# Performance work log

Hardware: AMD Instinct MI355X
Metric: run time of the kernel (lower is better)

The kernel has to match this reference:

```python
import jax, jax.numpy as jnp
import numpy as np

B, C, L, D = 8, 256, 2048, 128  # batch, in_channels, seq_len, n_factor


def setup_inputs() -> dict:
    key = jax.random.key(0)
    ks = jax.random.split(key, 8)
    s = 1.0 / np.sqrt(C)
    return {
        "x_inner": jax.random.normal(ks[0], (B, C, L), jnp.float32),
        "x_outer": jax.random.normal(ks[1], (B, C, L), jnp.float32),
        "Wq": jax.random.normal(ks[2], (D, C), jnp.float32) * s,
        "bq": jax.random.normal(ks[3], (D,), jnp.float32) * 0.01,
        "Wk": jax.random.normal(ks[4], (D, C), jnp.float32) * s,
        "bk": jax.random.normal(ks[5], (D,), jnp.float32) * 0.01,
        "Wv": jax.random.normal(ks[6], (D, C), jnp.float32) * s,
        "bv": jax.random.normal(ks[7], (D,), jnp.float32) * 0.01,
    }


def reference(x_inner, x_outer, Wq, bq, Wk, bk, Wv, bv):
    # kernel-size-1 Conv1d == per-position linear over channels; permute -> [B, L, D]
    q = jnp.einsum('bcl,dc->bld', x_inner, Wq) + bq  # [B, Lq, D]
    k = jnp.einsum('bcl,dc->bld', x_outer, Wk) + bk  # [B, Lk, D]
    v = jnp.einsum('bcl,dc->bld', x_outer, Wv) + bv  # [B, Lk, D]
    scores = jnp.einsum('bqd,bkd->bqk', q, k) / jnp.sqrt(jnp.asarray(D, q.dtype))
    attn = jax.nn.softmax(scores, axis=2)            # [B, Lq, Lk]
    return jnp.einsum('bqk,bkd->bqd', attn, v)       # [B, Lq, D]
```

## Files before the change

### kernel.cpp

```cpp
#include <hip/hip_runtime.h>
#include <hip/hip_bf16.h>

#define NB 8
#define NC 256
#define NL 2048
#define ND 128
#define NROWS (NB * NL)
#define QKV_ELEMS ((size_t)NB * NL * ND)
#define W_ELEMS (ND * NC)
#define XS_STRIDE 264

typedef __attribute__((ext_vector_type(8))) short bf16x8;
typedef __attribute__((ext_vector_type(4))) float f32x4;
typedef __attribute__((ext_vector_type(16))) float f32x16;
typedef __attribute__((ext_vector_type(4))) unsigned int u32x4;

__device__ __forceinline__ unsigned short f2bf(float f) {
    union { float f; unsigned u; } v; v.f = f;
    unsigned r = v.u + 0x7fffu + ((v.u >> 16) & 1u);
    return (unsigned short)(r >> 16);
}

__device__ __forceinline__ unsigned cvt_pk_bf16(float lo, float hi) {
    unsigned r;
    asm("v_cvt_pk_bf16_f32 %0, %1, %2" : "=v"(r) : "v"(lo), "v"(hi));
    return r;
}

__device__ __forceinline__ void pl32swap(unsigned &a, unsigned &b) {
    asm("v_permlane32_swap_b32 %0, %1" : "+v"(a), "+v"(b));
}

__device__ __forceinline__ void load_lds16(const unsigned short* g, unsigned short* l) {
    __builtin_amdgcn_global_load_lds((const __attribute__((address_space(1))) unsigned int*)g,
                                     (__attribute__((address_space(3))) unsigned int*)l, 16, 0, 0);
}

__global__ void cast_w3(const float* __restrict__ wq, const float* __restrict__ wk,
                        const float* __restrict__ wv, unsigned short* __restrict__ dst) {
    int i = blockIdx.x * blockDim.x + threadIdx.x;
    if (i >= 3 * W_ELEMS) return;
    int sel = i / W_ELEMS, off = i - sel * W_ELEMS;
    const float* s = (sel == 0) ? wq : (sel == 1) ? wk : wv;
    dst[i] = f2bf(s[off]);
}

__device__ __forceinline__ int xs_col(int row, int col) {
    return col ^ (((row >> 2) & 7) << 3);
}

__device__ __forceinline__ void qk_project(const unsigned short* xs, const unsigned short* Wb,
                                           const float* bias, unsigned short* out,
                                           int b, int l0, int wave, int ln, int quad) {
    int m0w = wave * 16;
    f32x4 acc[8] = {};
    int rowq = m0w + ln;
    #pragma unroll
    for (int s = 0; s < 8; s++) {
        bf16x8 af = *reinterpret_cast<const bf16x8*>(xs + rowq * XS_STRIDE + xs_col(rowq, s * 32 + quad * 8));
        #pragma unroll
        for (int t = 0; t < 8; t++) {
            bf16x8 bfr = *reinterpret_cast<const bf16x8*>(Wb + (size_t)(t * 16 + ln) * NC + s * 32 + quad * 8);
            acc[t] = __builtin_amdgcn_mfma_f32_16x16x32_bf16(af, bfr, acc[t], 0, 0, 0);
        }
    }
    #pragma unroll
    for (int t = 0; t < 8; t++) {
        int col = t * 16 + ln;
        float bi = bias[col];
        #pragma unroll
        for (int r = 0; r < 4; r++)
            out[(size_t)(b * NL + l0 + m0w + quad * 4 + r) * ND + col] = f2bf(acc[t][r] + bi);
    }
}

__global__ __launch_bounds__(256, 4) void proj_direct(const float* __restrict__ xi,
                                                      const float* __restrict__ xo,
                                                      const unsigned short* __restrict__ Wall,
                                                      const float* __restrict__ bq,
                                                      const float* __restrict__ bk,
                                                      const float* __restrict__ bv,
                                                      unsigned short* __restrict__ Qb,
                                                      unsigned short* __restrict__ Kb,
                                                      unsigned short* __restrict__ Vtb) {
    __shared__ unsigned short xs[64 * XS_STRIDE];
    int b = blockIdx.x >> 5, lt = blockIdx.x & 31, l0 = lt * 64;
    int y = blockIdx.y;
    int wave = threadIdx.x >> 6, lane = threadIdx.x & 63;
    int ln = lane & 15, quad = lane >> 4;

    const float* xsrc = (y == 0 ? xi : xo) + (size_t)b * NC * NL + l0;
    int l4 = ln * 4;
    #pragma unroll
    for (int G = 0; G < 4; G++) {
        int c0 = G * 64 + wave * 16 + quad * 4;
        float4 r[4];
        #pragma unroll
        for (int cc = 0; cc < 4; cc++)
            r[cc] = *reinterpret_cast<const float4*>(xsrc + (size_t)(c0 + cc) * NL + l4);
        #pragma unroll
        for (int k = 0; k < 4; k++) {
            int row = l4 + k;
            const float* f0 = reinterpret_cast<const float*>(&r[0]);
            const float* f1 = reinterpret_cast<const float*>(&r[1]);
            const float* f2 = reinterpret_cast<const float*>(&r[2]);
            const float* f3 = reinterpret_cast<const float*>(&r[3]);
            uint2 w2 = { cvt_pk_bf16(f0[k], f1[k]), cvt_pk_bf16(f2[k], f3[k]) };
            *reinterpret_cast<uint2*>(&xs[row * XS_STRIDE + xs_col(row, c0)]) = w2;
        }
    }
    __syncthreads();

    if (y == 0) {
        qk_project(xs, Wall, bq, Qb, b, l0, wave, ln, quad);
    } else {
        qk_project(xs, Wall + W_ELEMS, bk, Kb, b, l0, wave, ln, quad);
        const unsigned short* Wb = Wall + 2 * (size_t)W_ELEMS;
        f32x4 acc[2][4] = {};
        #pragma unroll
        for (int s = 0; s < 8; s++) {
            bf16x8 wf0 = *reinterpret_cast<const bf16x8*>(Wb + (size_t)(wave * 32 + ln) * NC + s * 32 + quad * 8);
            bf16x8 wf1 = *reinterpret_cast<const bf16x8*>(Wb + (size_t)(wave * 32 + 16 + ln) * NC + s * 32 + quad * 8);
            #pragma unroll
            for (int t = 0; t < 4; t++) {
                int rowv = t * 16 + ln;
                bf16x8 xb = *reinterpret_cast<const bf16x8*>(xs + rowv * XS_STRIDE + xs_col(rowv, s * 32 + quad * 8));
                acc[0][t] = __builtin_amdgcn_mfma_f32_16x16x32_bf16(wf0, xb, acc[0][t], 0, 0, 0);
                acc[1][t] = __builtin_amdgcn_mfma_f32_16x16x32_bf16(wf1, xb, acc[1][t], 0, 0, 0);
            }
        }
        #pragma unroll
        for (int u = 0; u < 2; u++)
            #pragma unroll
            for (int t = 0; t < 4; t++)
                #pragma unroll
                for (int r = 0; r < 4; r++) {
                    int d = wave * 32 + u * 16 + quad * 4 + r;
                    Vtb[(size_t)(b * ND + d) * NL + l0 + t * 16 + ln] = f2bf(acc[u][t][r] + bv[d]);
                }
    }
}

__global__ __launch_bounds__(256, 2) void flash_attn_s2(const unsigned short* __restrict__ Q,
                                                        const unsigned short* __restrict__ K,
                                                        const unsigned short* __restrict__ Vt,
                                                        float* __restrict__ Opart,
                                                        float* __restrict__ lbuf,
                                                        int kvlen) {
    __shared__ unsigned short kbuf[2][64 * 128];
    __shared__ unsigned short vbuf[2][128 * 64];
    int bx = blockIdx.x;
    bx = ((bx & 7) << 5) | (bx >> 3);
    int b = bx >> 5, qt = bx & 31;
    int q0 = qt * 64;
    int sp = blockIdx.y;
    int kv0 = sp * kvlen;
    int wave = threadIdx.x >> 6, lane = threadIdx.x & 63;
    int l31 = lane & 31, h = lane >> 5;
    int qg = wave >> 1, half = wave & 1;
    const float scale = 0.08838834764831845f * 1.4426950408889634f;

    bf16x8 qf[8];
    const unsigned short* qrow = Q + (size_t)(b * NL + q0 + qg * 32 + l31) * ND + h * 8;
    #pragma unroll
    for (int s = 0; s < 8; s++) qf[s] = *reinterpret_cast<const bf16x8*>(qrow + s * 16);

    float lsum = 0.f;
    f32x16 o_acc[4] = {};

    const unsigned short* kg = K + (size_t)b * NL * ND;
    const unsigned short* vg = Vt + (size_t)b * ND * NL;

    int krt = wave * 16 + (lane >> 4);
    int kjs = (lane & 15);
    int vdt = wave * 32 + (lane >> 3);
    int vjs = (lane & 7);

    #pragma unroll
    for (int i = 0; i < 4; i++) {
        int rt = krt + i * 4;
        load_lds16(kg + (size_t)(kv0 + rt) * ND + (kjs ^ (rt & 15)) * 8, kbuf[0] + (wave * 16 + i * 4) * 128);
    }
    #pragma unroll
    for (int i = 0; i < 4; i++) {
        int dt = vdt + i * 8;
        load_lds16(vg + (size_t)dt * NL + kv0 + (vjs ^ (dt & 7)) * 8, vbuf[0] + (wave * 32 + i * 8) * 64);
    }

    int niter = kvlen >> 6;
    for (int it = 0; it < niter; it++) {
        int cur = it & 1;
        __syncthreads();

        if (it + 1 < niter) {
            int kt = kv0 + (it + 1) * 64;
            int nxt = cur ^ 1;
            #pragma unroll
            for (int i = 0; i < 4; i++) {
                int rt = krt + i * 4;
                load_lds16(kg + (size_t)(kt + rt) * ND + (kjs ^ (rt & 15)) * 8, kbuf[nxt] + (wave * 16 + i * 4) * 128);
            }
            #pragma unroll
            for (int i = 0; i < 4; i++) {
                int dt = vdt + i * 8;
                load_lds16(vg + (size_t)dt * NL + kt + (vjs ^ (dt & 7)) * 8, vbuf[nxt] + (wave * 32 + i * 8) * 64);
            }
        }
        const unsigned short* kb = kbuf[cur];
        const unsigned short* vb = vbuf[cur];

        f32x16 sacc0 = {}, sacc1 = {};
        __builtin_amdgcn_s_setprio(1);
        {
            const unsigned short* krow_p = kb + (half * 32 + l31) * 128;
            #pragma unroll
            for (int s = 0; s < 8; s += 2) {
                bf16x8 kf0 = *reinterpret_cast<const bf16x8*>(krow_p + ((((s + 0) * 2 + h) ^ (l31 & 15)) << 3));
                bf16x8 kf1 = *reinterpret_cast<const bf16x8*>(krow_p + ((((s + 1) * 2 + h) ^ (l31 & 15)) << 3));
                sacc0 = __builtin_amdgcn_mfma_f32_32x32x16_bf16(kf0, qf[s], sacc0, 0, 0, 0);
                sacc1 = __builtin_amdgcn_mfma_f32_32x32x16_bf16(kf1, qf[s + 1], sacc1, 0, 0, 0);
            }
        }
        __builtin_amdgcn_s_setprio(0);

        float p[16];
        #pragma unroll
        for (int g = 0; g < 16; g++) p[g] = __builtin_exp2f((sacc0[g] + sacc1[g]) * scale);
        lsum += (((p[0] + p[1]) + (p[2] + p[3])) + ((p[4] + p[5]) + (p[6] + p[7])))
              + (((p[8] + p[9]) + (p[10] + p[11])) + ((p[12] + p[13]) + (p[14] + p[15])));
        unsigned c0 = cvt_pk_bf16(p[0], p[1]),   c1 = cvt_pk_bf16(p[2], p[3]);
        unsigned c2 = cvt_pk_bf16(p[4], p[5]),   c3 = cvt_pk_bf16(p[6], p[7]);
        unsigned c4 = cvt_pk_bf16(p[8], p[9]),   c5 = cvt_pk_bf16(p[10], p[11]);
        unsigned c6 = cvt_pk_bf16(p[12], p[13]), c7 = cvt_pk_bf16(p[14], p[15]);
        pl32swap(c0, c2); pl32swap(c1, c3);
        pl32swap(c4, c6); pl32swap(c5, c7);
        u32x4 wlo = {c0, c1, c2, c3};
        u32x4 whi = {c4, c5, c6, c7};
        bf16x8 pb0 = __builtin_bit_cast(bf16x8, wlo);
        bf16x8 pb1 = __builtin_bit_cast(bf16x8, whi);

        __builtin_amdgcn_s_setprio(1);
        #pragma unroll
        for (int dt = 0; dt < 4; dt++) {
            const unsigned short* vrow = vb + (dt * 32 + l31) * 64;
            int s0 = half * 2;
            bf16x8 vf0 = *reinterpret_cast<const bf16x8*>(vrow + ((((s0 + 0) * 2 + h) ^ (l31 & 7)) << 3));
            bf16x8 vf1 = *reinterpret_cast<const bf16x8*>(vrow + ((((s0 + 1) * 2 + h) ^ (l31 & 7)) << 3));
            o_acc[dt] = __builtin_amdgcn_mfma_f32_32x32x16_bf16(vf0, pb0, o_acc[dt], 0, 0, 0);
            o_acc[dt] = __builtin_amdgcn_mfma_f32_32x32x16_bf16(vf1, pb1, o_acc[dt], 0, 0, 0);
        }
        __builtin_amdgcn_s_setprio(0);
    }
    lsum += __shfl_xor(lsum, 32);

    __syncthreads();
    float* ored = reinterpret_cast<float*>(&kbuf[0][0]);
    float* lred = reinterpret_cast<float*>(&vbuf[0][0]);
    if (half == 1) {
        float* o = ored + qg * (128 * 32);
        #pragma unroll
        for (int dt = 0; dt < 4; dt++)
            #pragma unroll
            for (int g = 0; g < 4; g++)
                #pragma unroll
                for (int r = 0; r < 4; r++)
                    o[(dt * 32 + g * 8 + h * 4 + r) * 32 + l31] = o_acc[dt][g * 4 + r];
        if (lane < 32) lred[qg * 32 + l31] = lsum;
    }
    __syncthreads();
    if (half == 0) {
        float* o = ored + qg * (128 * 32);
        float Lt = lsum + lred[qg * 32 + l31];
        int qrow_g = b * NL + q0 + qg * 32 + l31;
        if (lane < 32) lbuf[(size_t)sp * NROWS + qrow_g] = Lt;
        float* op = Opart + (size_t)sp * QKV_ELEMS;
        #pragma unroll
        for (int dt = 0; dt < 4; dt++) {
            #pragma unroll
            for (int g = 0; g < 4; g++) {
                f32x4 v4;
                #pragma unroll
                for (int r = 0; r < 4; r++)
                    v4[r] = o_acc[dt][g * 4 + r] + o[(dt * 32 + g * 8 + h * 4 + r) * 32 + l31];
                *reinterpret_cast<f32x4*>(op + (size_t)qrow_g * ND + dt * 32 + g * 8 + h * 4) = v4;
            }
        }
    }
}

__global__ __launch_bounds__(256) void attn_merge(const float* __restrict__ Opart,
                                                  const float* __restrict__ lbuf,
                                                  float* __restrict__ out, int S) {
    int idx = blockIdx.x * 256 + threadIdx.x;
    int row = idx >> 5;
    int dg = (idx & 31) * 4;
    float L = 0.f;
    float4 acc = make_float4(0.f, 0.f, 0.f, 0.f);
    for (int s = 0; s < S; s++) {
        L += lbuf[(size_t)s * NROWS + row];
        float4 o = *reinterpret_cast<const float4*>(Opart + (size_t)s * QKV_ELEMS + (size_t)row * ND + dg);
        acc.x += o.x; acc.y += o.y; acc.z += o.z; acc.w += o.w;
    }
    float inv = 1.0f / L;
    float4 res = make_float4(acc.x * inv, acc.y * inv, acc.z * inv, acc.w * inv);
    *reinterpret_cast<float4*>(out + (size_t)row * ND + dg) = res;
}

extern "C" void kernel_launch(void* const* d_in, const int* in_sizes, int n_in,
                              void* d_out, int out_size, void* d_ws, size_t ws_size,
                              hipStream_t stream) {
    const float* x_inner = (const float*)d_in[0];
    const float* x_outer = (const float*)d_in[1];
    const float* Wq = (const float*)d_in[2];
    const float* bq = (const float*)d_in[3];
    const float* Wk = (const float*)d_in[4];
    const float* bk = (const float*)d_in[5];
    const float* Wv = (const float*)d_in[6];
    const float* bv = (const float*)d_in[7];
    float* out = (float*)d_out;

    const int S = 2;
    char* w = (char*)d_ws;
    float* Opart = (float*)w;
    float* lbuf = (float*)(w + (size_t)S * QKV_ELEMS * 4);
    char* w2 = w + (size_t)S * QKV_ELEMS * 4 + (size_t)S * NROWS * 4;
    unsigned short* Qb = (unsigned short*)w2;
    unsigned short* Kb = Qb + QKV_ELEMS;
    unsigned short* Vtb = Kb + QKV_ELEMS;
    unsigned short* Wall = Vtb + QKV_ELEMS;

    cast_w3<<<(3 * W_ELEMS + 255) / 256, 256, 0, stream>>>(Wq, Wk, Wv, Wall);
    dim3 pgrid(NB * (NL / 64), 2);
    proj_direct<<<pgrid, 256, 0, stream>>>(x_inner, x_outer, Wall, bq, bk, bv, Qb, Kb, Vtb);
    dim3 fgrid(NB * (NL / 64), S);
    flash_attn_s2<<<fgrid, 256, 0, stream>>>(Qb, Kb, Vtb, Opart, lbuf, NL / S);
    attn_merge<<<(NROWS * ND / 4 + 255) / 256, 256, 0, stream>>>(Opart, lbuf, out, S);
}
```

Before: 149.0 us.

## Fuse split-KV merge into attention kernel via last-arriver atomic counter

Removes the separate attn_merge kernel. Each attention block writes its partial output and row sums, then bumps a per-tile atomic counter. The second block to arrive reads the other split's partial, normalizes, and writes the final output. The counters are zeroed in the weight-cast kernel. This saves one kernel launch and a full pass over both partial buffers, at the cost of thread fences, an atomic, and extra tail work in the last-arriving blocks.

After: 211.8 us. 42.2% more time.

```diff
diff --git a/kernel.cpp b/kernel.cpp
--- a/kernel.cpp
+++ b/kernel.cpp
@@ -37,8 +37,10 @@
 }
 
 __global__ void cast_w3(const float* __restrict__ wq, const float* __restrict__ wk,
-                        const float* __restrict__ wv, unsigned short* __restrict__ dst) {
+                        const float* __restrict__ wv, unsigned short* __restrict__ dst,
+                        int* __restrict__ cnt) {
     int i = blockIdx.x * blockDim.x + threadIdx.x;
+    if (i < 256) cnt[i] = 0;
     if (i >= 3 * W_ELEMS) return;
     int sel = i / W_ELEMS, off = i - sel * W_ELEMS;
     const float* s = (sel == 0) ? wq : (sel == 1) ? wk : wv;
@@ -146,11 +148,14 @@
                                                         const unsigned short* __restrict__ Vt,
                                                         float* __restrict__ Opart,
                                                         float* __restrict__ lbuf,
+                                                        int* __restrict__ cnt,
+                                                        float* __restrict__ out,
                                                         int kvlen) {
     __shared__ unsigned short kbuf[2][64 * 128];
     __shared__ unsigned short vbuf[2][128 * 64];
-    int bx = blockIdx.x;
-    bx = ((bx & 7) << 5) | (bx >> 3);
+    __shared__ int sOld;
+    int bx_orig = blockIdx.x;
+    int bx = ((bx_orig & 7) << 5) | (bx_orig >> 3);
     int b = bx >> 5, qt = bx & 31;
     int q0 = qt * 64;
     int sp = blockIdx.y;
@@ -268,42 +273,52 @@
         if (lane < 32) lred[qg * 32 + l31] = lsum;
     }
     __syncthreads();
+    int qrow_g = b * NL + q0 + qg * 32 + l31;
+    float Lt = 0.f;
     if (half == 0) {
         float* o = ored + qg * (128 * 32);
-        float Lt = lsum + lred[qg * 32 + l31];
-        int qrow_g = b * NL + q0 + qg * 32 + l31;
+        #pragma unroll
+        for (int dt = 0; dt < 4; dt++)
+            #pragma unroll
+            for (int g = 0; g < 4; g++)
+                #pragma unroll
+                for (int r = 0; r < 4; r++)
+                    o_acc[dt][g * 4 + r] += o[(dt * 32 + g * 8 + h * 4 + r) * 32 + l31];
+        Lt = lsum + lred[qg * 32 + l31];
         if (lane < 32) lbuf[(size_t)sp * NROWS + qrow_g] = Lt;
         float* op = Opart + (size_t)sp * QKV_ELEMS;
         #pragma unroll
         for (int dt = 0; dt < 4; dt++) {
             #pragma unroll
             for (int g = 0; g < 4; g++) {
+                f32x4 v4 = { o_acc[dt][g * 4 + 0], o_acc[dt][g * 4 + 1],
+                             o_acc[dt][g * 4 + 2], o_acc[dt][g * 4 + 3] };
+                *reinterpret_cast<f32x4*>(op + (size_t)qrow_g * ND + dt * 32 + g * 8 + h * 4) = v4;
+            }
+        }
+    }
+    __threadfence();
+    __syncthreads();
+    if (threadIdx.x == 0) sOld = atomicAdd(cnt + bx_orig, 1);
+    __syncthreads();
+    if (sOld == 1 && half == 0) {
+        __threadfence();
+        float Lo = lbuf[(size_t)(sp ^ 1) * NROWS + qrow_g];
+        float inv = 1.0f / (Lt + Lo);
+        const float* op = Opart + (size_t)(sp ^ 1) * QKV_ELEMS;
+        #pragma unroll
+        for (int dt = 0; dt < 4; dt++) {
+            #pragma unroll
+            for (int g = 0; g < 4; g++) {
+                f32x4 pv = *reinterpret_cast<const f32x4*>(op + (size_t)qrow_g * ND + dt * 32 + g * 8 + h * 4);
                 f32x4 v4;
                 #pragma unroll
                 for (int r = 0; r < 4; r++)
-                    v4[r] = o_acc[dt][g * 4 + r] + o[(dt * 32 + g * 8 + h * 4 + r) * 32 + l31];
-                *reinterpret_cast<f32x4*>(op + (size_t)qrow_g * ND + dt * 32 + g * 8 + h * 4) = v4;
-            }
-        }
-    }
-}
-
-__global__ __launch_bounds__(256) void attn_merge(const float* __restrict__ Opart,
-                                                  const float* __restrict__ lbuf,
-                                                  float* __restrict__ out, int S) {
-    int idx = blockIdx.x * 256 + threadIdx.x;
-    int row = idx >> 5;
-    int dg = (idx & 31) * 4;
-    float L = 0.f;
-    float4 acc = make_float4(0.f, 0.f, 0.f, 0.f);
-    for (int s = 0; s < S; s++) {
-        L += lbuf[(size_t)s * NROWS + row];
-        float4 o = *reinterpret_cast<const float4*>(Opart + (size_t)s * QKV_ELEMS + (size_t)row * ND + dg);
-        acc.x += o.x; acc.y += o.y; acc.z += o.z; acc.w += o.w;
-    }
-    float inv = 1.0f / L;
-    float4 res = make_float4(acc.x * inv, acc.y * inv, acc.z * inv, acc.w * inv);
-    *reinterpret_cast<float4*>(out + (size_t)row * ND + dg) = res;
+                    v4[r] = (o_acc[dt][g * 4 + r] + pv[r]) * inv;
+                *reinterpret_cast<f32x4*>(out + (size_t)qrow_g * ND + dt * 32 + g * 8 + h * 4) = v4;
+            }
+        }
+    }
 }
 
 extern "C" void kernel_launch(void* const* d_in, const int* in_sizes, int n_in,
@@ -328,11 +343,11 @@
     unsigned short* Kb = Qb + QKV_ELEMS;
     unsigned short* Vtb = Kb + QKV_ELEMS;
     unsigned short* Wall = Vtb + QKV_ELEMS;
-
-    cast_w3<<<(3 * W_ELEMS + 255) / 256, 256, 0, stream>>>(Wq, Wk, Wv, Wall);
+    int* cnt = (int*)(Wall + 3 * W_ELEMS);
+
+    cast_w3<<<(3 * W_ELEMS + 255) / 256, 256, 0, stream>>>(Wq, Wk, Wv, Wall, cnt);
     dim3 pgrid(NB * (NL / 64), 2);
     proj_direct<<<pgrid, 256, 0, stream>>>(x_inner, x_outer, Wall, bq, bk, bv, Qb, Kb, Vtb);
     dim3 fgrid(NB * (NL / 64), S);
-    flash_attn_s2<<<fgrid, 256, 0, stream>>>(Qb, Kb, Vtb, Opart, lbuf, NL / S);
-    attn_merge<<<(NROWS * ND / 4 + 255) / 256, 256, 0, stream>>>(Opart, lbuf, out, S);
-}
+    flash_attn_s2<<<fgrid, 256, 0, stream>>>(Qb, Kb, Vtb, Opart, lbuf, cnt, out, NL / S);
+}
```
